# Optimization experiments

Measured on AMD Instinct MI355X. Metric: run time of the kernel, lower is better.

Reference implementation:

```python
import jax, jax.numpy as jnp
import numpy as np

N_NODES = 500_000
N_EDGES = 16_000_000
D_COEF = 1  # init arg d
EPS = 1e-12  # F.normalize eps


def setup_inputs() -> dict:
    key = jax.random.key(0)
    k1, k2, k3 = jax.random.split(key, 3)
    theta = jax.random.normal(k1, (N_NODES, 1), dtype=jnp.float32)
    src = jax.random.randint(k2, (N_EDGES,), 0, N_NODES, dtype=jnp.int64)
    dst = jax.random.randint(k3, (N_EDGES,), 0, N_NODES, dtype=jnp.int64)
    v0 = jnp.ones((), dtype=jnp.float32)
    w0 = jnp.ones((), dtype=jnp.float32)
    return {"theta": theta, "src": src, "dst": dst, "v0": v0, "w0": w0}


def reference(theta, src, dst, v0, w0):
    # node velocity: v0 * [cos(theta), sin(theta)]  -> [N, 2]
    v = v0 * jnp.concatenate((jnp.cos(theta), jnp.sin(theta)), axis=-1)

    # edge message: dtheta = (theta_src - theta_dst) * d ; m = [cos, sin] -> [E, 2]
    dtheta = (theta[src, 0] - theta[dst, 0]) * D_COEF  # [E]
    m = jnp.stack((jnp.cos(dtheta), jnp.sin(dtheta)), axis=-1)  # [E, 2]

    # mailbox mean over incoming edges per destination node (segment mean)
    msum = jax.ops.segment_sum(m, dst, num_segments=N_NODES)  # [N, 2]
    cnt = jax.ops.segment_sum(jnp.ones((dst.shape[0],), m.dtype), dst,
                              num_segments=N_NODES)  # [N]
    mean_cs = msum / jnp.maximum(cnt, 1.0)[:, None]  # [N, 2]

    # torque: w0 * normalize(mean_cs, dim=-1)[..., 1:2]
    norm = jnp.linalg.norm(mean_cs, axis=-1, keepdims=True)
    unit = mean_cs / jnp.maximum(norm, EPS)
    torque = w0 * unit[:, 1:2]  # [N, 1]
    return v, torque
```

## Files before the change

### kernel.cpp

```cpp
#include <hip/hip_runtime.h>
#include <hip/hip_bf16.h>
#include <math.h>


#define NBITS_Q   21
#define Q_MASK    ((1u << NBITS_Q) - 1)
#define Q_SCALE   131072.0f
#define Q_INV     (1.0f / 131072.0f)
#define BIN_SHIFT 11
#define BIN_W     2048
#define NB        245
#define CAP       67584
#define K_BATCH   8192
#define EPT       32
#define SCALE_F   524288.0f
#define INV_SCALE (1.0f / 524288.0f)

__global__ void init_cursors(unsigned* __restrict__ cur) {
    int b = blockIdx.x * blockDim.x + threadIdx.x;
    if (b < 256) cur[b] = (b < NB) ? (unsigned)b * CAP : 0u;
}

__global__ __launch_bounds__(256) void bin_edges_sort(
        const float* __restrict__ theta,
        const int4* __restrict__ src4, const int4* __restrict__ dst4,
        unsigned* __restrict__ bins, unsigned* __restrict__ cursor, int E)
{
    __shared__ unsigned      sorted[K_BATCH];
    __shared__ unsigned char sbin[K_BATCH];
    __shared__ unsigned      hist[256];
    __shared__ unsigned      base[256];
    __shared__ unsigned      gbase[256];
    __shared__ unsigned      lcnt[256];

    const int tid   = threadIdx.x;
    const int bb    = blockIdx.x;
    const int e0    = bb * K_BATCH;
    const int nval  = min(K_BATCH, E - e0);
    const int E4    = E >> 2;
    const int base4 = e0 >> 2;

    hist[tid] = 0;
    lcnt[tid] = 0;
    __syncthreads();

    int4 sQ[EPT / 4];
#pragma unroll
    for (int j = 0; j < EPT / 4; ++j) {
        const int idx4 = base4 + j * 256 + tid;
        sQ[j] = (idx4 < E4) ? src4[idx4] : make_int4(0, 0, 0, 0);
    }
    float tq[EPT];
#pragma unroll
    for (int j = 0; j < EPT / 4; ++j) {
        tq[j * 4 + 0] = theta[sQ[j].x];
        tq[j * 4 + 1] = theta[sQ[j].y];
        tq[j * 4 + 2] = theta[sQ[j].z];
        tq[j * 4 + 3] = theta[sQ[j].w];
    }

    unsigned ent[EPT];
    unsigned bn[EPT];
#pragma unroll
    for (int j = 0; j < EPT / 4; ++j) {
        const int idx4 = base4 + j * 256 + tid;
        const int q0   = j * 4;
        if (idx4 < E4) {
            const int4 d = dst4[idx4];
            const int dd[4] = {d.x, d.y, d.z, d.w};
#pragma unroll
            for (int k = 0; k < 4; ++k) {
                const unsigned b = (unsigned)dd[k] >> BIN_SHIFT;
                float qf = (tq[q0 + k] + 8.0f) * Q_SCALE + 0.5f;
                qf = fminf(fmaxf(qf, 0.0f), 2097151.0f);
                ent[q0 + k] = ((unsigned)(dd[k] & (BIN_W - 1)) << NBITS_Q)
                              | (unsigned)qf;
                bn[q0 + k]  = b;
                atomicAdd(&hist[b], 1u);
            }
        } else {
#pragma unroll
            for (int k = 0; k < 4; ++k) bn[q0 + k] = 0xFFu;
        }
    }
    __syncthreads();

    const unsigned x = hist[tid];
    base[tid] = x;
    __syncthreads();
    for (int off = 1; off < 256; off <<= 1) {
        const unsigned y = (tid >= off) ? base[tid - off] : 0u;
        __syncthreads();
        base[tid] += y;
        __syncthreads();
    }
    const unsigned excl = base[tid] - x;
    __syncthreads();
    base[tid] = excl;
    if (x) gbase[tid] = atomicAdd(&cursor[tid], x);
    __syncthreads();

#pragma unroll
    for (int q = 0; q < EPT; ++q) {
        if (bn[q] != 0xFFu) {
            const unsigned b   = bn[q];
            const unsigned pos = base[b] + atomicAdd(&lcnt[b], 1u);
            sorted[pos] = ent[q];
            sbin[pos]   = (unsigned char)b;
        }
    }
    __syncthreads();

    for (int l = tid; l < nval; l += 256) {
        const unsigned b    = sbin[l];
        const unsigned gpos = gbase[b] + ((unsigned)l - base[b]);
        if (gpos < (b + 1u) * CAP)
            bins[gpos] = sorted[l];
    }
}

__global__ __launch_bounds__(1024) void reduce_bins(
        const float* __restrict__ theta, const unsigned* __restrict__ bins,
        const unsigned* __restrict__ cursor, const float* __restrict__ v0p,
        const float* __restrict__ w0p, float* __restrict__ out, int N)
{
    __shared__ float th[BIN_W];
    __shared__ unsigned long long acc[BIN_W];
    const int b     = blockIdx.x;
    const int tid   = threadIdx.x;
    const int node0 = b * BIN_W;
    const int W     = min(BIN_W, N - node0);

    for (int j = tid; j < BIN_W; j += 1024) {
        th[j]  = (j < W) ? theta[node0 + j] : 0.f;
        acc[j] = 0ull;
    }
    __syncthreads();

    const unsigned  base  = (unsigned)b * CAP;
    const int       count = (int)(cursor[b] - base);
    const unsigned* bp    = bins + base;

    const int CH = 1024 * 8;
    int i0 = 0;
    for (; i0 + CH <= count; i0 += CH) {
        const uint4 ea = *(const uint4*)(bp + i0 + tid * 4);
        const uint4 eb = *(const uint4*)(bp + i0 + 4096 + tid * 4);
        const unsigned ee[8] = {ea.x, ea.y, ea.z, ea.w, eb.x, eb.y, eb.z, eb.w};
#pragma unroll
        for (int k = 0; k < 8; ++k) {
            const unsigned e = ee[k];
            const unsigned l = e >> NBITS_Q;
            const float ts = (float)(e & Q_MASK) * Q_INV - 8.0f;
            float sn, cs;
            __sincosf(ts - th[l], &sn, &cs);
            const unsigned cq = (unsigned)((cs + 1.0f) * SCALE_F + 0.5f);
            const unsigned sq = (unsigned)((sn + 1.0f) * SCALE_F + 0.5f);
            atomicAdd(&acc[l], (1ull << 56) | ((unsigned long long)cq << 28)
                               | (unsigned long long)sq);
        }
    }
    for (int i = i0 + tid; i < count; i += 1024) {
        const unsigned e = bp[i];
        const unsigned l = e >> NBITS_Q;
        const float ts = (float)(e & Q_MASK) * Q_INV - 8.0f;
        float sn, cs;
        __sincosf(ts - th[l], &sn, &cs);
        const unsigned cq = (unsigned)((cs + 1.0f) * SCALE_F + 0.5f);
        const unsigned sq = (unsigned)((sn + 1.0f) * SCALE_F + 0.5f);
        atomicAdd(&acc[l], (1ull << 56) | ((unsigned long long)cq << 28)
                           | (unsigned long long)sq);
    }
    __syncthreads();

    const float v0 = *v0p, w0 = *w0p;
    for (int j = tid; j < W; j += 1024) {
        const float t = th[j];
        float sn, cs;
        __sincosf(t, &sn, &cs);
        ((float2*)out)[node0 + j] = make_float2(v0 * cs, v0 * sn);
        const unsigned long long P = acc[j];
        const float c  = (float)(unsigned)(P >> 56);
        const float xs = (float)(unsigned)((P >> 28) & 0xFFFFFFFull) * INV_SCALE - c;
        const float ys = (float)(unsigned)(P & 0xFFFFFFFull) * INV_SCALE - c;
        const float nrm = sqrtf(xs * xs + ys * ys);
        out[2 * N + node0 + j] = w0 * (ys / fmaxf(nrm, 1e-12f));
    }
}


__global__ void zero_ws_kernel(float4* __restrict__ ws, int n4) {
    int i = blockIdx.x * blockDim.x + threadIdx.x;
    if (i < n4) ws[i] = make_float4(0.f, 0.f, 0.f, 0.f);
}

__global__ void edge_kernel_fb(const float* __restrict__ theta,
                               const int4* __restrict__ src4,
                               const int4* __restrict__ dst4,
                               float2* __restrict__ acc, int E8) {
    int i = blockIdx.x * blockDim.x + threadIdx.x;
    if (i >= E8) return;
    const int4 s0 = src4[2 * i], s1 = src4[2 * i + 1];
    const int4 d0 = dst4[2 * i], d1 = dst4[2 * i + 1];
    const int ss[8] = {s0.x, s0.y, s0.z, s0.w, s1.x, s1.y, s1.z, s1.w};
    const int dd[8] = {d0.x, d0.y, d0.z, d0.w, d1.x, d1.y, d1.z, d1.w};
    float ts[8], td[8];
#pragma unroll
    for (int k = 0; k < 8; ++k) ts[k] = theta[ss[k]];
#pragma unroll
    for (int k = 0; k < 8; ++k) td[k] = theta[dd[k]];
#pragma unroll
    for (int k = 0; k < 8; ++k) {
        float sn, cs;
        __sincosf(ts[k] - td[k], &sn, &cs);
        atomicAdd(&acc[dd[k]].x, cs);
        atomicAdd(&acc[dd[k]].y, sn);
    }
}

__global__ void node_kernel_fb(const float* __restrict__ theta,
                               const float2* __restrict__ acc,
                               const float* __restrict__ v0p,
                               const float* __restrict__ w0p,
                               float* __restrict__ out, int N) {
    int i = blockIdx.x * blockDim.x + threadIdx.x;
    if (i >= N) return;
    const float v0 = *v0p, w0 = *w0p;
    float sn, cs;
    __sincosf(theta[i], &sn, &cs);
    ((float2*)out)[i] = make_float2(v0 * cs, v0 * sn);
    const float2 a = acc[i];
    const float nrm = sqrtf(a.x * a.x + a.y * a.y);
    out[2 * N + i] = w0 * (a.y / fmaxf(nrm, 1e-12f));
}

extern "C" void kernel_launch(void* const* d_in, const int* in_sizes, int n_in,
                              void* d_out, int out_size, void* d_ws, size_t ws_size,
                              hipStream_t stream) {
    const float* theta = (const float*)d_in[0];
    const int*   src   = (const int*)d_in[1];
    const int*   dst   = (const int*)d_in[2];
    const float* v0p   = (const float*)d_in[3];
    const float* w0p   = (const float*)d_in[4];
    float*       out   = (float*)d_out;

    const int N = in_sizes[0];
    const int E = in_sizes[1];

    const size_t need = 1024 + (size_t)NB * CAP * sizeof(unsigned);

    if (ws_size >= need && N <= NB * BIN_W) {
        unsigned* cursor = (unsigned*)d_ws;
        unsigned* bins   = cursor + 256;

        init_cursors<<<1, 256, 0, stream>>>(cursor);

        const int nblk = (E + K_BATCH - 1) / K_BATCH;
        bin_edges_sort<<<nblk, 256, 0, stream>>>(theta, (const int4*)src,
                                                 (const int4*)dst,
                                                 bins, cursor, E);

        const int nbins = (N + BIN_W - 1) / BIN_W;
        reduce_bins<<<nbins, 1024, 0, stream>>>(theta, bins, cursor,
                                                v0p, w0p, out, N);
    } else {
        float2* acc = (float2*)d_ws;
        {
            const int n4 = (2 * N) / 4;
            zero_ws_kernel<<<(n4 + 255) / 256, 256, 0, stream>>>((float4*)d_ws, n4);
        }
        {
            const int E8 = E / 8;
            edge_kernel_fb<<<(E8 + 255) / 256, 256, 0, stream>>>(
                theta, (const int4*)src, (const int4*)dst, acc, E8);
        }
        node_kernel_fb<<<(N + 255) / 256, 256, 0, stream>>>(theta, acc, v0p, w0p,
                                                            out, N);
    }
}
```

Measured before the change: 264.5 us.

## Use 1024-thread blocks with 8 edges per thread and wave-shuffle histogram scan

The binning kernel now runs 1024 threads per block, each handling 8 edges instead of 32, so the per-thread register arrays shrink and each batch is spread over more threads. The dst index load is hoisted next to the src load so both are in flight together. The 256-entry exclusive scan, previously a barrier-heavy shared-memory loop, is replaced by a single-wave shuffle scan over 4 entries per lane. The cost is more threads contending on the shared histogram and local-cursor atomics within each block.

Measured after the change: 304.5 us. +15.1%, slower.

```diff
diff --git a/kernel.cpp b/kernel.cpp
--- a/kernel.cpp
+++ b/kernel.cpp
@@ -12,7 +12,7 @@
 #define NB        245
 #define CAP       67584
 #define K_BATCH   8192
-#define EPT       32
+#define EPT       8
 #define SCALE_F   524288.0f
 #define INV_SCALE (1.0f / 524288.0f)
 
@@ -21,7 +21,7 @@
     if (b < 256) cur[b] = (b < NB) ? (unsigned)b * CAP : 0u;
 }
 
-__global__ __launch_bounds__(256) void bin_edges_sort(
+__global__ __launch_bounds__(1024, 8) void bin_edges_sort(
         const float* __restrict__ theta,
         const int4* __restrict__ src4, const int4* __restrict__ dst4,
         unsigned* __restrict__ bins, unsigned* __restrict__ cursor, int E)
@@ -40,15 +40,20 @@
     const int E4    = E >> 2;
     const int base4 = e0 >> 2;
 
-    hist[tid] = 0;
-    lcnt[tid] = 0;
-    __syncthreads();
-
-    int4 sQ[EPT / 4];
+    if (tid < 256) { hist[tid] = 0u; lcnt[tid] = 0u; }
+    __syncthreads();
+
+    int4 sQ[EPT / 4], dQ[EPT / 4];
 #pragma unroll
     for (int j = 0; j < EPT / 4; ++j) {
-        const int idx4 = base4 + j * 256 + tid;
-        sQ[j] = (idx4 < E4) ? src4[idx4] : make_int4(0, 0, 0, 0);
+        const int idx4 = base4 + j * 1024 + tid;
+        if (idx4 < E4) {
+            sQ[j] = src4[idx4];
+            dQ[j] = dst4[idx4];
+        } else {
+            sQ[j] = make_int4(0, 0, 0, 0);
+            dQ[j] = make_int4(0, 0, 0, 0);
+        }
     }
     float tq[EPT];
 #pragma unroll
@@ -63,11 +68,10 @@
     unsigned bn[EPT];
 #pragma unroll
     for (int j = 0; j < EPT / 4; ++j) {
-        const int idx4 = base4 + j * 256 + tid;
+        const int idx4 = base4 + j * 1024 + tid;
         const int q0   = j * 4;
         if (idx4 < E4) {
-            const int4 d = dst4[idx4];
-            const int dd[4] = {d.x, d.y, d.z, d.w};
+            const int dd[4] = {dQ[j].x, dQ[j].y, dQ[j].z, dQ[j].w};
 #pragma unroll
             for (int k = 0; k < 4; ++k) {
                 const unsigned b = (unsigned)dd[k] >> BIN_SHIFT;
@@ -85,19 +89,27 @@
     }
     __syncthreads();
 
-    const unsigned x = hist[tid];
-    base[tid] = x;
-    __syncthreads();
-    for (int off = 1; off < 256; off <<= 1) {
-        const unsigned y = (tid >= off) ? base[tid - off] : 0u;
-        __syncthreads();
-        base[tid] += y;
-        __syncthreads();
-    }
-    const unsigned excl = base[tid] - x;
-    __syncthreads();
-    base[tid] = excl;
-    if (x) gbase[tid] = atomicAdd(&cursor[tid], x);
+    if (tid < 64) {
+        unsigned h[4];
+#pragma unroll
+        for (int k = 0; k < 4; ++k) h[k] = hist[tid * 4 + k];
+        const unsigned tot = h[0] + h[1] + h[2] + h[3];
+        unsigned s = tot;
+#pragma unroll
+        for (int off = 1; off < 64; off <<= 1) {
+            const unsigned y = __shfl_up(s, off);
+            if (tid >= off) s += y;
+        }
+        unsigned run = s - tot;
+#pragma unroll
+        for (int k = 0; k < 4; ++k) {
+            base[tid * 4 + k] = run;
+            run += h[k];
+        }
+#pragma unroll
+        for (int k = 0; k < 4; ++k)
+            if (h[k]) gbase[tid * 4 + k] = atomicAdd(&cursor[tid * 4 + k], h[k]);
+    }
     __syncthreads();
 
 #pragma unroll
@@ -111,7 +123,7 @@
     }
     __syncthreads();
 
-    for (int l = tid; l < nval; l += 256) {
+    for (int l = tid; l < nval; l += 1024) {
         const unsigned b    = sbin[l];
         const unsigned gpos = gbase[b] + ((unsigned)l - base[b]);
         if (gpos < (b + 1u) * CAP)
@@ -256,9 +268,9 @@
         init_cursors<<<1, 256, 0, stream>>>(cursor);
 
         const int nblk = (E + K_BATCH - 1) / K_BATCH;
-        bin_edges_sort<<<nblk, 256, 0, stream>>>(theta, (const int4*)src,
-                                                 (const int4*)dst,
-                                                 bins, cursor, E);
+        bin_edges_sort<<<nblk, 1024, 0, stream>>>(theta, (const int4*)src,
+                                                  (const int4*)dst,
+                                                  bins, cursor, E);
 
         const int nbins = (N + BIN_W - 1) / BIN_W;
         reduce_bins<<<nbins, 1024, 0, stream>>>(theta, bins, cursor,
```
